# Kernel optimization log

Hardware: AMD Instinct MI355X
Metric: run time of the kernel (lower is better)

Reference implementation:

```python
import jax, jax.numpy as jnp
import numpy as np

N = 256
DT = 1.0 / 4096.0
BATCH = 256
LENGTH = 4096

def _legt_transition(n):
    # HiPPO-LegT continuous-time transition (Gu et al.)
    Q = np.arange(n, dtype=np.float64)
    R = (2.0 * Q + 1.0) ** 0.5
    j, i = np.meshgrid(Q, Q)
    A = R[:, None] * np.where(i < j, (-1.0) ** (i - j), 1.0) * R[None, :]
    B = R[:, None]
    return -A, B

def _bilinear(A, B, dt):
    # scipy cont2discrete(method='bilinear'), alpha=0.5
    n = A.shape[0]
    ima = np.eye(n) - 0.5 * dt * A
    Ad = np.linalg.solve(ima, np.eye(n) + 0.5 * dt * A)
    Bd = np.linalg.solve(ima, dt * B)
    return Ad, Bd

def setup_inputs() -> dict:
    key = jax.random.key(0)
    Ac, Bc = _legt_transition(N)
    evals = (2.0 * np.arange(N, dtype=np.float64) + 1.0) ** 0.5
    C = evals @ Ac                        # (N,) readout from continuous A
    D = np.sum(evals * Bc.squeeze(-1))    # scalar
    scale = 1.0 / (1.0 - 0.5 * D * DT)
    C_discr = (scale * 0.5 * DT * C).astype(np.float32)          # (N,)
    D_discr = np.array([scale * (1.0 + 0.5 * DT * D)], np.float32)  # (1,)
    Ad, Bd = _bilinear(Ac, Bc, DT)
    inputs = jax.random.normal(key, (BATCH, LENGTH), dtype=jnp.float32)
    return {
        "inputs": inputs,
        "A": jnp.asarray(Ad, dtype=jnp.float32),
        "B": jnp.asarray(Bd.squeeze(-1), dtype=jnp.float32),
        "C_discr": jnp.asarray(C_discr),
        "D_discr": jnp.asarray(D_discr),
    }

def reference(inputs, A, B, C_discr, D_discr):
    # inputs: (batch, length). teacher_ratio=1.0 -> fully teacher-forced LTI scan:
    #   c_t = A c_{t-1} + B * u_t ;  pred_t = fac_t * (c_t @ C) + D * u_t
    # where fac_0 = 1 and fac_t = 2 for t > 0 (as in the torch loop).
    batch, length = inputs.shape
    c0 = jnp.zeros((batch, A.shape[0]), dtype=inputs.dtype)
    facs = jnp.where(jnp.arange(length) == 0, 1.0, 2.0).astype(inputs.dtype)

    def step(c, xs):
        x_t, fac = xs                                   # x_t: (batch,)
        c = c @ A.T + B[None, :] * x_t[:, None]         # (batch, N); F.linear(c, A)
        pred = fac * (c @ C_discr) + D_discr[0] * x_t   # (batch,)
        return c, pred

    _, preds = jax.lax.scan(step, c0, (inputs.T, facs))  # preds: (length, batch)
    return preds.T  # (batch, length)
```

## Files before the change

### kernel.cpp

```cpp
#include <hip/hip_runtime.h>


#define LENGTH 4096

#define WS_P2    0
#define WS_P4    65536
#define WS_P8    131072
#define WS_P16   196608
#define WS_P32   262144
#define WS_P64T  327680
#define WS_P128T 393216
#define WS_W     458752
#define WS_V     475136
#define WS_K     491520
#define WS_XH    495616
#define WS_XL    1019904
#define WS_AH    1544192
#define WS_AL    1609728

typedef __attribute__((ext_vector_type(8))) short bf16x8;
typedef __attribute__((ext_vector_type(4))) float f32x4;
#define MFMA(a, b, c) __builtin_amdgcn_mfma_f32_16x16x32_bf16(a, b, c, 0, 0, 0)

__device__ inline unsigned short f2bf(float f) {
    unsigned int u = __float_as_uint(f);
    return (unsigned short)((u + 0x7FFFu + ((u >> 16) & 1u)) >> 16);
}
__device__ inline void split2(float f, short& h, short& l) {
    unsigned short hu = f2bf(f);
    float fh = __uint_as_float((unsigned int)hu << 16);
    h = (short)hu;
    l = (short)f2bf(f - fh);
}

__global__ __launch_bounds__(1024) void mmrow(const float* __restrict__ X,
                                              const float* __restrict__ Y,
                                              float* __restrict__ Z) {
    const int i = blockIdx.x, t = threadIdx.x;
    const int j = t & 255, p = t >> 8;
    __shared__ float red[3][256];
    const float* xr = X + i * 256 + 64 * p;
    const float* yc = Y + (64 * p) * 256 + j;
    float a0 = 0.f, a1 = 0.f, a2 = 0.f, a3 = 0.f;
#pragma unroll
    for (int l = 0; l < 64; l += 4) {
        a0 = fmaf(xr[l + 0], yc[(l + 0) * 256], a0);
        a1 = fmaf(xr[l + 1], yc[(l + 1) * 256], a1);
        a2 = fmaf(xr[l + 2], yc[(l + 2) * 256], a2);
        a3 = fmaf(xr[l + 3], yc[(l + 3) * 256], a3);
    }
    float s = (a0 + a1) + (a2 + a3);
    if (p) red[p - 1][j] = s;
    __syncthreads();
    if (p == 0) Z[i * 256 + j] = s + red[0][j] + red[1][j] + red[2][j];
}

__global__ __launch_bounds__(1024) void mm2(const float* __restrict__ P32,
                                            float* __restrict__ P64T) {
    const int i = blockIdx.x, t = threadIdx.x;
    const int j = t & 255, p = t >> 8;
    __shared__ float red[3][256];
    const float* xr = P32 + i * 256 + 64 * p;
    const float* yc = P32 + (64 * p) * 256 + j;
    float a0 = 0.f, a1 = 0.f, a2 = 0.f, a3 = 0.f;
#pragma unroll
    for (int l = 0; l < 64; l += 4) {
        a0 = fmaf(xr[l + 0], yc[(l + 0) * 256], a0);
        a1 = fmaf(xr[l + 1], yc[(l + 1) * 256], a1);
        a2 = fmaf(xr[l + 2], yc[(l + 2) * 256], a2);
        a3 = fmaf(xr[l + 3], yc[(l + 3) * 256], a3);
    }
    float s = (a0 + a1) + (a2 + a3);
    if (p) red[p - 1][j] = s;
    __syncthreads();
    if (p == 0) P64T[j * 256 + i] = s + red[0][j] + red[1][j] + red[2][j];
}

__global__ __launch_bounds__(1024) void wvgen(const float* __restrict__ A,
                                              const float* __restrict__ B,
                                              const float* __restrict__ C,
                                              const float* __restrict__ P32,
                                              const float* __restrict__ P64T,
                                              const float* __restrict__ P128T,
                                              float* __restrict__ W,
                                              float* __restrict__ V) {
    const int t = threadIdx.x;
    const int bid = blockIdx.x;
    const int j = t & 255, p = t >> 8;
    __shared__ float cur[256];
    __shared__ float red[4][256];

    if (bid < 2) {
        float areg[64];
#pragma unroll
        for (int ii = 0; ii < 64; ++ii) areg[ii] = A[(64 * p + ii) * 256 + j];

        if (bid == 0) {
            if (t < 256) cur[t] = C[t];
            __syncthreads();
        } else {
            float s0 = 0.f, s1 = 0.f, s2 = 0.f, s3 = 0.f;
#pragma unroll 4
            for (int ii = 0; ii < 64; ii += 4) {
                s0 = fmaf(C[64 * p + ii + 0], P32[(64 * p + ii + 0) * 256 + j], s0);
                s1 = fmaf(C[64 * p + ii + 1], P32[(64 * p + ii + 1) * 256 + j], s1);
                s2 = fmaf(C[64 * p + ii + 2], P32[(64 * p + ii + 2) * 256 + j], s2);
                s3 = fmaf(C[64 * p + ii + 3], P32[(64 * p + ii + 3) * 256 + j], s3);
            }
            red[p][j] = (s0 + s1) + (s2 + s3);
            __syncthreads();
            if (p == 0) cur[j] = red[0][j] + red[1][j] + red[2][j] + red[3][j];
            __syncthreads();
        }
        const int base = bid * 32;
        if (p == 0) W[base * 256 + j] = cur[j];
        for (int r = 1; r < 32; ++r) {
            float s0 = 0.f, s1 = 0.f, s2 = 0.f, s3 = 0.f;
#pragma unroll
            for (int m = 0; m < 16; ++m) {
                float4 c4 = *reinterpret_cast<const float4*>(&cur[64 * p + 4 * m]);
                s0 = fmaf(c4.x, areg[4 * m + 0], s0);
                s1 = fmaf(c4.y, areg[4 * m + 1], s1);
                s2 = fmaf(c4.z, areg[4 * m + 2], s2);
                s3 = fmaf(c4.w, areg[4 * m + 3], s3);
            }
            red[p][j] = (s0 + s1) + (s2 + s3);
            __syncthreads();
            if (p == 0) {
                float s = red[0][j] + red[1][j] + red[2][j] + red[3][j];
                cur[j] = s;
                W[(base + r) * 256 + j] = s;
            }
            __syncthreads();
        }
    } else {
        const int i = j;
        float mreg[64];
#pragma unroll
        for (int jj = 0; jj < 64; ++jj) mreg[jj] = P128T[(64 * p + jj) * 256 + i];
        if (t < 256) cur[t] = B[t];
        __syncthreads();

        if (bid == 3) {
            float s0 = 0.f, s1 = 0.f, s2 = 0.f, s3 = 0.f;
#pragma unroll 4
            for (int jj = 0; jj < 64; jj += 4) {
                s0 = fmaf(P64T[(64 * p + jj + 0) * 256 + i], cur[64 * p + jj + 0], s0);
                s1 = fmaf(P64T[(64 * p + jj + 1) * 256 + i], cur[64 * p + jj + 1], s1);
                s2 = fmaf(P64T[(64 * p + jj + 2) * 256 + i], cur[64 * p + jj + 2], s2);
                s3 = fmaf(P64T[(64 * p + jj + 3) * 256 + i], cur[64 * p + jj + 3], s3);
            }
            red[p][i] = (s0 + s1) + (s2 + s3);
            __syncthreads();
            if (p == 0) cur[i] = red[0][i] + red[1][i] + red[2][i] + red[3][i];
            __syncthreads();
        }
        const int off = bid - 2;
        for (int m = 0; m < 32; ++m) {
            if (p == 0) V[(2 * m + off) * 256 + i] = cur[i];
            if (m == 31) break;
            float s0 = 0.f, s1 = 0.f, s2 = 0.f, s3 = 0.f;
#pragma unroll
            for (int mm = 0; mm < 16; ++mm) {
                float4 c4 = *reinterpret_cast<const float4*>(&cur[64 * p + 4 * mm]);
                s0 = fmaf(c4.x, mreg[4 * mm + 0], s0);
                s1 = fmaf(c4.y, mreg[4 * mm + 1], s1);
                s2 = fmaf(c4.z, mreg[4 * mm + 2], s2);
                s3 = fmaf(c4.w, mreg[4 * mm + 3], s3);
            }
            red[p][i] = (s0 + s1) + (s2 + s3);
            __syncthreads();
            if (p == 0) cur[i] = red[0][i] + red[1][i] + red[2][i] + red[3][i];
            __syncthreads();
        }
    }
}

__global__ __launch_bounds__(256) void kdot(const float* __restrict__ W,
                                            const float* __restrict__ V,
                                            float* __restrict__ K) {
    const int q = blockIdx.x, tid = threadIdx.x;
    const int r = tid & 63, p = tid >> 6;
    __shared__ float Wl[64 * 257];
    __shared__ float Vl[256];
    __shared__ float red[4][64];
    for (int u = 0; u < 64; ++u) Wl[u * 257 + tid] = W[u * 256 + tid];
    Vl[tid] = V[q * 256 + tid];
    __syncthreads();
    float s0 = 0.f, s1 = 0.f;
#pragma unroll
    for (int m = 0; m < 64; m += 2) {
        s0 = fmaf(Wl[r * 257 + 64 * p + m + 0], Vl[64 * p + m + 0], s0);
        s1 = fmaf(Wl[r * 257 + 64 * p + m + 1], Vl[64 * p + m + 1], s1);
    }
    red[p][r] = s0 + s1;
    __syncthreads();
    if (tid < 64) K[q * 64 + tid] = red[0][tid] + red[1][tid] + red[2][tid] + red[3][tid];
}

__global__ __launch_bounds__(256) void xsplit(const float* __restrict__ x,
                                              short* __restrict__ XH,
                                              short* __restrict__ XL) {
    const int w = threadIdx.x >> 6, lane = threadIdx.x & 63;
    const int p = blockIdx.x * 4 + w;
    const int c = p >> 4, blk = p & 15;
    const int b = blk * 16 + (lane & 15);
    const int s0 = c * 32 + 8 * (lane >> 4);
    const float4 v0 = reinterpret_cast<const float4*>(&x[b * LENGTH + s0])[0];
    const float4 v1 = reinterpret_cast<const float4*>(&x[b * LENGTH + s0])[1];
    const float f[8] = {v0.x, v0.y, v0.z, v0.w, v1.x, v1.y, v1.z, v1.w};
    bf16x8 hv, lv;
#pragma unroll
    for (int e = 0; e < 8; ++e) {
        short h, l;
        split2(f[e], h, l);
        hv[e] = h; lv[e] = l;
    }
    const int off = (p * 64 + lane) * 8;
    *reinterpret_cast<bf16x8*>(XH + off) = hv;
    *reinterpret_cast<bf16x8*>(XL + off) = lv;
}

__global__ __launch_bounds__(256) void afrag(const float* __restrict__ K,
                                             short* __restrict__ AH,
                                             short* __restrict__ AL) {
    const int m = blockIdx.x * 4 + (threadIdx.x >> 6);
    const int lane = threadIdx.x & 63;
    bf16x8 hv, lv;
#pragma unroll
    for (int e = 0; e < 8; ++e) {
        const int kidx = 16 * m + (lane & 15) - 8 * (lane >> 4) - e;
        const float kv = (kidx >= 0) ? K[kidx] : 0.f;
        short h, l;
        split2(kv, h, l);
        hv[e] = h; lv[e] = l;
    }
    const int off = (m * 64 + lane) * 8;
    *reinterpret_cast<bf16x8*>(AH + off) = hv;
    *reinterpret_cast<bf16x8*>(AL + off) = lv;
}

struct Frag {
    bf16x8 bh0, bh1, bl0, bl1;
    bf16x8 ah0, ah1, ah2, ah3, al0, al1, al2, al3;
    int d0, tile;
};

__global__ __launch_bounds__(512) void convm(const short* __restrict__ XH,
                                             const short* __restrict__ XL,
                                             const short* __restrict__ AH,
                                             const short* __restrict__ AL,
                                             const float* __restrict__ x,
                                             const float* __restrict__ Dp,
                                             float* __restrict__ out) {
    const int pr = blockIdx.x & 31;
    const int bt = blockIdx.x >> 5;
    const int tid = threadIdx.x;
    const int w = tid >> 6, lane = tid & 63;
    const int tA64 = pr * 64, tB64 = (63 - pr) * 64;
    const int nA = 2 * pr + 2;
    const int bt2 = bt * 2;

    __shared__ float lds[16 * 64 * 34];

    f32x4 acc[2][4][2];
#pragma unroll
    for (int t_ = 0; t_ < 2; ++t_)
#pragma unroll
        for (int r_ = 0; r_ < 4; ++r_)
#pragma unroll
            for (int c_ = 0; c_ < 2; ++c_) acc[t_][r_][c_] = f32x4{0.f, 0.f, 0.f, 0.f};

#define LOADF(F, IDX_) do {                                                    \
        const int i_ = (IDX_);                                                 \
        const int tl_ = (i_ < nA) ? 0 : 1;                                     \
        const int cc_ = i_ - (tl_ ? nA : 0);                                   \
        const int xo_ = ((cc_ * 16 + bt2) * 64 + lane) * 8;                    \
        F.bh0 = *reinterpret_cast<const bf16x8*>(XH + xo_);                    \
        F.bh1 = *reinterpret_cast<const bf16x8*>(XH + xo_ + 512);              \
        F.bl0 = *reinterpret_cast<const bf16x8*>(XL + xo_);                    \
        F.bl1 = *reinterpret_cast<const bf16x8*>(XL + xo_ + 512);              \
        const int d_ = (tl_ ? tB64 : tA64) - cc_ * 32;                         \
        F.d0 = d_; F.tile = tl_;                                               \
        const int m0_ = (d_ > 0 ? d_ : 0) >> 4;                                \
        const int m1_ = (d_ + 16 > 0 ? d_ + 16 : 0) >> 4;                      \
        const int m2_ = (d_ + 32 > 0 ? d_ + 32 : 0) >> 4;                      \
        const int m3_ = (d_ + 48 > 0 ? d_ + 48 : 0) >> 4;                      \
        F.ah0 = *reinterpret_cast<const bf16x8*>(AH + (m0_ * 64 + lane) * 8);  \
        F.al0 = *reinterpret_cast<const bf16x8*>(AL + (m0_ * 64 + lane) * 8);  \
        F.ah1 = *reinterpret_cast<const bf16x8*>(AH + (m1_ * 64 + lane) * 8);  \
        F.al1 = *reinterpret_cast<const bf16x8*>(AL + (m1_ * 64 + lane) * 8);  \
        F.ah2 = *reinterpret_cast<const bf16x8*>(AH + (m2_ * 64 + lane) * 8);  \
        F.al2 = *reinterpret_cast<const bf16x8*>(AL + (m2_ * 64 + lane) * 8);  \
        F.ah3 = *reinterpret_cast<const bf16x8*>(AH + (m3_ * 64 + lane) * 8);  \
        F.al3 = *reinterpret_cast<const bf16x8*>(AL + (m3_ * 64 + lane) * 8);  \
    } while (0)

#define ONER(F, T, R, AHF, ALF)                                                \
        if (F.d0 + 16 * R >= 0) {                                              \
            acc[T][R][0] = MFMA(F.AHF, F.bh0, acc[T][R][0]);                   \
            acc[T][R][1] = MFMA(F.AHF, F.bh1, acc[T][R][1]);                   \
            acc[T][R][0] = MFMA(F.AHF, F.bl0, acc[T][R][0]);                   \
            acc[T][R][1] = MFMA(F.AHF, F.bl1, acc[T][R][1]);                   \
            acc[T][R][0] = MFMA(F.ALF, F.bh0, acc[T][R][0]);                   \
            acc[T][R][1] = MFMA(F.ALF, F.bh1, acc[T][R][1]);                   \
        }

#define APPLY(F) do {                                                          \
        if (F.tile == 0) {                                                     \
            ONER(F, 0, 0, ah0, al0) ONER(F, 0, 1, ah1, al1)                    \
            ONER(F, 0, 2, ah2, al2) ONER(F, 0, 3, ah3, al3)                    \
        } else {                                                               \
            ONER(F, 1, 0, ah0, al0) ONER(F, 1, 1, ah1, al1)                    \
            ONER(F, 1, 2, ah2, al2) ONER(F, 1, 3, ah3, al3)                    \
        }                                                                      \
    } while (0)

    Frag f0, f1;
    LOADF(f0, w);
    int idx = w;
    while (true) {
        const int n1 = idx + 8;
        const bool h1 = n1 < 130;
        if (h1) LOADF(f1, n1);
        APPLY(f0);
        if (!h1) break;
        const int n2 = n1 + 8;
        const bool h2 = n2 < 130;
        if (h2) LOADF(f0, n2);
        APPLY(f1);
        if (!h2) break;
        idx = n2;
    }

    const int lq = lane >> 4, lr = lane & 15;
#pragma unroll
    for (int t_ = 0; t_ < 2; ++t_)
#pragma unroll
        for (int r_ = 0; r_ < 4; ++r_)
#pragma unroll
            for (int c_ = 0; c_ < 2; ++c_)
#pragma unroll
                for (int e_ = 0; e_ < 4; ++e_)
                    lds[((w * 2 + t_) * 64 + (r_ * 16 + lq * 4 + e_)) * 34 +
                        (c_ * 16 + lr)] = acc[t_][r_][c_][e_];
    __syncthreads();

    const float D = Dp[0];
    const int b = tid >> 4;
    const int t4 = (tid & 15) * 4;
#pragma unroll
    for (int t_ = 0; t_ < 2; ++t_) {
        const int tbase = t_ ? tB64 : tA64;
        float s0 = 0.f, s1 = 0.f, s2 = 0.f, s3 = 0.f;
#pragma unroll
        for (int w_ = 0; w_ < 8; ++w_) {
            const float* lp = &lds[((w_ * 2 + t_) * 64 + t4) * 34 + b];
            s0 += lp[0]; s1 += lp[34]; s2 += lp[68]; s3 += lp[102];
        }
        const int g = (bt * 32 + b) * LENGTH + tbase + t4;
        const float4 xv = *reinterpret_cast<const float4*>(x + g);
        float4 o;
        o.x = 2.f * s0 + D * xv.x;
        o.y = 2.f * s1 + D * xv.y;
        o.z = 2.f * s2 + D * xv.z;
        o.w = 2.f * s3 + D * xv.w;
        if (tbase == 0 && t4 == 0) o.x -= s0;
        *reinterpret_cast<float4*>(out + g) = o;
    }
}

extern "C" void kernel_launch(void* const* d_in, const int* in_sizes, int n_in,
                              void* d_out, int out_size, void* d_ws, size_t ws_size,
                              hipStream_t stream) {
    const float* x  = (const float*)d_in[0];
    const float* A  = (const float*)d_in[1];
    const float* B  = (const float*)d_in[2];
    const float* C  = (const float*)d_in[3];
    const float* Dp = (const float*)d_in[4];
    float* out = (float*)d_out;
    float* ws  = (float*)d_ws;

    float* P2    = ws + WS_P2;
    float* P4    = ws + WS_P4;
    float* P8    = ws + WS_P8;
    float* P16   = ws + WS_P16;
    float* P32   = ws + WS_P32;
    float* P64T  = ws + WS_P64T;
    float* P128T = ws + WS_P128T;
    float* Wm    = ws + WS_W;
    float* Vm    = ws + WS_V;
    float* K     = ws + WS_K;
    short* XHs   = (short*)(ws + WS_XH);
    short* XLs   = (short*)(ws + WS_XL);
    short* AHs   = (short*)(ws + WS_AH);
    short* ALs   = (short*)(ws + WS_AL);

    xsplit<<<512, 256, 0, stream>>>(x, XHs, XLs);
    mmrow<<<256, 1024, 0, stream>>>(A, A, P2);
    mmrow<<<256, 1024, 0, stream>>>(P2, P2, P4);
    mmrow<<<256, 1024, 0, stream>>>(P4, P4, P8);
    mmrow<<<256, 1024, 0, stream>>>(P8, P8, P16);
    mmrow<<<256, 1024, 0, stream>>>(P16, P16, P32);
    mm2<<<256, 1024, 0, stream>>>(P32, P64T);
    mmrow<<<256, 1024, 0, stream>>>(P64T, P64T, P128T);
    wvgen<<<4, 1024, 0, stream>>>(A, B, C, P32, P64T, P128T, Wm, Vm);
    kdot<<<64, 256, 0, stream>>>(Wm, Vm, K);
    afrag<<<64, 256, 0, stream>>>(K, AHs, ALs);
    convm<<<256, 512, 0, stream>>>(XHs, XLs, AHs, ALs, x, Dp, out);
}
```

Before: 103.8 us.

## Fuse kernel-generation pipeline into one cooperative kernel with grid syncs

Replaces the chain of eleven small launches (xsplit, repeated squaring matmuls, wvgen, kdot, afrag) with one cooperative kernel of 256 blocks that separates phases with grid.sync. If cooperative launch fails it falls back to per-phase launches. It also reworks the W/V generation to use 16-step chains across 4 blocks with an extra P256 power, overlapping that work with the P128/P256 squarings. K computation and fragment packing are fused so K no longer goes through global memory. The aim is to remove launch overhead and serialised low-occupancy phases, at the cost of grid barrier latency and one large kernel with heavy register and shared-memory use.

```diff
diff --git a/kernel.cpp b/kernel.cpp
--- a/kernel.cpp
+++ b/kernel.cpp
@@ -1,4 +1,7 @@
 #include <hip/hip_runtime.h>
+#include <hip/hip_cooperative_groups.h>
+
+namespace cg = cooperative_groups;
 
 
 #define LENGTH 4096
@@ -10,13 +13,13 @@
 #define WS_P32   262144
 #define WS_P64T  327680
 #define WS_P128T 393216
-#define WS_W     458752
-#define WS_V     475136
-#define WS_K     491520
-#define WS_XH    495616
-#define WS_XL    1019904
-#define WS_AH    1544192
-#define WS_AL    1609728
+#define WS_P256T 458752
+#define WS_W     524288
+#define WS_V     540672
+#define WS_XH    557056
+#define WS_XL    1081344
+#define WS_AH    1605632
+#define WS_AL    1671168
 
 typedef __attribute__((ext_vector_type(8))) short bf16x8;
 typedef __attribute__((ext_vector_type(4))) float f32x4;
@@ -33,13 +36,12 @@
     l = (short)f2bf(f - fh);
 }
 
-__global__ __launch_bounds__(1024) void mmrow(const float* __restrict__ X,
-                                              const float* __restrict__ Y,
-                                              float* __restrict__ Z) {
-    const int i = blockIdx.x, t = threadIdx.x;
+__device__ __forceinline__ void mm_body(const float* __restrict__ X,
+                                        const float* __restrict__ Y,
+                                        float* __restrict__ Z,
+                                        int row, int t, bool trans, float* red) {
     const int j = t & 255, p = t >> 8;
-    __shared__ float red[3][256];
-    const float* xr = X + i * 256 + 64 * p;
+    const float* xr = X + row * 256 + 64 * p;
     const float* yc = Y + (64 * p) * 256 + j;
     float a0 = 0.f, a1 = 0.f, a2 = 0.f, a3 = 0.f;
 #pragma unroll
@@ -50,194 +52,255 @@
         a3 = fmaf(xr[l + 3], yc[(l + 3) * 256], a3);
     }
     float s = (a0 + a1) + (a2 + a3);
-    if (p) red[p - 1][j] = s;
-    __syncthreads();
-    if (p == 0) Z[i * 256 + j] = s + red[0][j] + red[1][j] + red[2][j];
-}
-
-__global__ __launch_bounds__(1024) void mm2(const float* __restrict__ P32,
-                                            float* __restrict__ P64T) {
-    const int i = blockIdx.x, t = threadIdx.x;
+    __syncthreads();
+    if (p) red[(p - 1) * 256 + j] = s;
+    __syncthreads();
+    if (!p) {
+        float z = s + red[j] + red[256 + j] + red[512 + j];
+        if (trans) Z[j * 256 + row] = z;
+        else       Z[row * 256 + j] = z;
+    }
+}
+
+__device__ __forceinline__ void rv_mm(const float* __restrict__ v,
+                                      const float* __restrict__ M,
+                                      float* curl, float* red4, int j, int p) {
+    float s0 = 0.f, s1 = 0.f;
+#pragma unroll
+    for (int ii = 0; ii < 64; ii += 2) {
+        s0 = fmaf(v[64 * p + ii],     M[(64 * p + ii) * 256 + j],     s0);
+        s1 = fmaf(v[64 * p + ii + 1], M[(64 * p + ii + 1) * 256 + j], s1);
+    }
+    red4[p * 256 + j] = s0 + s1;
+    __syncthreads();
+    if (!p) curl[j] = red4[j] + red4[256 + j] + red4[512 + j] + red4[768 + j];
+    __syncthreads();
+}
+
+__device__ __forceinline__ void cv_mm(const float* __restrict__ MT,
+                                      const float* __restrict__ v,
+                                      float* curl, float* red4, int i, int p) {
+    float s0 = 0.f, s1 = 0.f;
+#pragma unroll
+    for (int jj = 0; jj < 64; jj += 2) {
+        s0 = fmaf(MT[(64 * p + jj) * 256 + i],     v[64 * p + jj],     s0);
+        s1 = fmaf(MT[(64 * p + jj + 1) * 256 + i], v[64 * p + jj + 1], s1);
+    }
+    red4[p * 256 + i] = s0 + s1;
+    __syncthreads();
+    if (!p) curl[i] = red4[i] + red4[256 + i] + red4[512 + i] + red4[768 + i];
+    __syncthreads();
+}
+
+__global__ __launch_bounds__(1024) void genk(const float* __restrict__ x,
+                                             const float* __restrict__ A,
+                                             const float* __restrict__ B,
+                                             const float* __restrict__ C,
+                                             float* __restrict__ ws,
+                                             int ph) {
+    const bool coop = (ph < 0);
+    cg::grid_group grid = cg::this_grid();
+    const int bid = blockIdx.x;
+    const int t = threadIdx.x;
     const int j = t & 255, p = t >> 8;
-    __shared__ float red[3][256];
-    const float* xr = P32 + i * 256 + 64 * p;
-    const float* yc = P32 + (64 * p) * 256 + j;
-    float a0 = 0.f, a1 = 0.f, a2 = 0.f, a3 = 0.f;
-#pragma unroll
-    for (int l = 0; l < 64; l += 4) {
-        a0 = fmaf(xr[l + 0], yc[(l + 0) * 256], a0);
-        a1 = fmaf(xr[l + 1], yc[(l + 1) * 256], a1);
-        a2 = fmaf(xr[l + 2], yc[(l + 2) * 256], a2);
-        a3 = fmaf(xr[l + 3], yc[(l + 3) * 256], a3);
-    }
-    float s = (a0 + a1) + (a2 + a3);
-    if (p) red[p - 1][j] = s;
-    __syncthreads();
-    if (p == 0) P64T[j * 256 + i] = s + red[0][j] + red[1][j] + red[2][j];
-}
-
-__global__ __launch_bounds__(1024) void wvgen(const float* __restrict__ A,
-                                              const float* __restrict__ B,
-                                              const float* __restrict__ C,
-                                              const float* __restrict__ P32,
-                                              const float* __restrict__ P64T,
-                                              const float* __restrict__ P128T,
-                                              float* __restrict__ W,
-                                              float* __restrict__ V) {
-    const int t = threadIdx.x;
-    const int bid = blockIdx.x;
-    const int j = t & 255, p = t >> 8;
-    __shared__ float cur[256];
-    __shared__ float red[4][256];
-
-    if (bid < 2) {
-        float areg[64];
-#pragma unroll
-        for (int ii = 0; ii < 64; ++ii) areg[ii] = A[(64 * p + ii) * 256 + j];
-
-        if (bid == 0) {
-            if (t < 256) cur[t] = C[t];
+
+    __shared__ __align__(16) float shm[17376];
+    float* red  = shm;
+    float* curl = shm + 1024;
+    float* red4 = shm + 1280;
+
+    float* P2    = ws + WS_P2;
+    float* P4    = ws + WS_P4;
+    float* P8    = ws + WS_P8;
+    float* P16   = ws + WS_P16;
+    float* P32   = ws + WS_P32;
+    float* P64T  = ws + WS_P64T;
+    float* P128T = ws + WS_P128T;
+    float* P256T = ws + WS_P256T;
+    float* Wm    = ws + WS_W;
+    float* Vm    = ws + WS_V;
+    short* XH    = (short*)(ws + WS_XH);
+    short* XL    = (short*)(ws + WS_XL);
+    short* AH    = (short*)(ws + WS_AH);
+    short* AL    = (short*)(ws + WS_AL);
+
+    if (coop || ph == 0) {
+        mm_body(A, A, P2, bid, t, false, red);
+        const int wv = t >> 6, lane = t & 63;
+        if (wv < 8) {
+            const int pj = bid * 8 + wv;
+            const int c = pj >> 4, blk = pj & 15;
+            const int b = blk * 16 + (lane & 15);
+            const int s0 = c * 32 + 8 * (lane >> 4);
+            const float4 v0 = reinterpret_cast<const float4*>(&x[b * LENGTH + s0])[0];
+            const float4 v1 = reinterpret_cast<const float4*>(&x[b * LENGTH + s0])[1];
+            const float f[8] = {v0.x, v0.y, v0.z, v0.w, v1.x, v1.y, v1.z, v1.w};
+            bf16x8 hv, lv;
+#pragma unroll
+            for (int e = 0; e < 8; ++e) {
+                short h_, l_;
+                split2(f[e], h_, l_);
+                hv[e] = h_; lv[e] = l_;
+            }
+            const int off = (pj * 64 + lane) * 8;
+            *reinterpret_cast<bf16x8*>(XH + off) = hv;
+            *reinterpret_cast<bf16x8*>(XL + off) = lv;
+        }
+    }
+    if (coop) grid.sync();
+    if (coop || ph == 1) mm_body(P2, P2, P4, bid, t, false, red);
+    if (coop) grid.sync();
+    if (coop || ph == 2) mm_body(P4, P4, P8, bid, t, false, red);
+    if (coop) grid.sync();
+    if (coop || ph == 3) mm_body(P8, P8, P16, bid, t, false, red);
+    if (coop) grid.sync();
+    if (coop || ph == 4) mm_body(P16, P16, P32, bid, t, false, red);
+    if (coop) grid.sync();
+    if (coop || ph == 5) mm_body(P32, P32, P64T, bid, t, true, red);
+    if (coop) grid.sync();
+
+    if (coop || ph == 6) {
+        if (bid >= 4) {
+            mm_body(P64T, P64T, P128T, bid - 4, t, false, red);
+            if (bid < 8) mm_body(P64T, P64T, P128T, 248 + bid, t, false, red);
+        } else {
+            const int c = bid;
+            float areg[64];
+#pragma unroll
+            for (int ii = 0; ii < 64; ++ii) areg[ii] = A[(64 * p + ii) * 256 + j];
+            if (c == 0) {
+                if (t < 256) curl[t] = C[t];
+                __syncthreads();
+            } else {
+                rv_mm(C, (c == 2) ? P32 : P16, curl, red4, j, p);
+                if (c == 3) rv_mm(curl, P32, curl, red4, j, p);
+            }
+            for (int s_ = 0; s_ < 16; ++s_) {
+                if (!p) Wm[(16 * c + s_) * 256 + j] = curl[j];
+                if (s_ == 15) break;
+                float s0 = 0.f, s1 = 0.f;
+#pragma unroll
+                for (int m = 0; m < 16; ++m) {
+                    float4 c4 = *reinterpret_cast<const float4*>(&curl[64 * p + 4 * m]);
+                    s0 = fmaf(c4.x, areg[4 * m + 0], s0);
+                    s1 = fmaf(c4.y, areg[4 * m + 1], s1);
+                    s0 = fmaf(c4.z, areg[4 * m + 2], s0);
+                    s1 = fmaf(c4.w, areg[4 * m + 3], s1);
+                }
+                red4[p * 256 + j] = s0 + s1;
+                __syncthreads();
+                if (!p) curl[j] = red4[j] + red4[256 + j] + red4[512 + j] + red4[768 + j];
+                __syncthreads();
+            }
+        }
+    }
+    if (coop) grid.sync();
+
+    if (coop || ph == 7) {
+        if (bid >= 4) {
+            mm_body(P128T, P128T, P256T, bid - 4, t, false, red);
+            if (bid < 8) mm_body(P128T, P128T, P256T, 248 + bid, t, false, red);
+        } else {
+            const int c = bid;
+            if (c == 0) {
+                if (t < 256) Vm[t] = B[t];
+            } else if (c == 1) {
+                cv_mm(P64T, B, curl, red4, j, p);
+                if (!p) Vm[256 + j] = curl[j];
+            } else if (c == 2) {
+                cv_mm(P128T, B, curl, red4, j, p);
+                if (!p) Vm[512 + j] = curl[j];
+            } else {
+                cv_mm(P128T, B, curl, red4, j, p);
+                cv_mm(P64T, curl, curl, red4, j, p);
+                if (!p) Vm[768 + j] = curl[j];
+            }
+        }
+    }
+    if (coop) grid.sync();
+
+    if (coop || ph == 8) {
+        if (bid < 4) {
+            const int c = bid, i = j;
+            if (t < 256) curl[t] = Vm[c * 256 + t];
             __syncthreads();
-        } else {
-            float s0 = 0.f, s1 = 0.f, s2 = 0.f, s3 = 0.f;
-#pragma unroll 4
-            for (int ii = 0; ii < 64; ii += 4) {
-                s0 = fmaf(C[64 * p + ii + 0], P32[(64 * p + ii + 0) * 256 + j], s0);
-                s1 = fmaf(C[64 * p + ii + 1], P32[(64 * p + ii + 1) * 256 + j], s1);
-                s2 = fmaf(C[64 * p + ii + 2], P32[(64 * p + ii + 2) * 256 + j], s2);
-                s3 = fmaf(C[64 * p + ii + 3], P32[(64 * p + ii + 3) * 256 + j], s3);
-            }
-            red[p][j] = (s0 + s1) + (s2 + s3);
+            float mreg[64];
+#pragma unroll
+            for (int jj = 0; jj < 64; ++jj) mreg[jj] = P256T[(64 * p + jj) * 256 + i];
+            for (int s_ = 1; s_ < 16; ++s_) {
+                float s0 = 0.f, s1 = 0.f;
+#pragma unroll
+                for (int m = 0; m < 16; ++m) {
+                    float4 c4 = *reinterpret_cast<const float4*>(&curl[64 * p + 4 * m]);
+                    s0 = fmaf(c4.x, mreg[4 * m + 0], s0);
+                    s1 = fmaf(c4.y, mreg[4 * m + 1], s1);
+                    s0 = fmaf(c4.z, mreg[4 * m + 2], s0);
+                    s1 = fmaf(c4.w, mreg[4 * m + 3], s1);
+                }
+                red4[p * 256 + i] = s0 + s1;
+                __syncthreads();
+                if (!p) {
+                    float s = red4[i] + red4[256 + i] + red4[512 + i] + red4[768 + i];
+                    curl[i] = s;
+                    Vm[(4 * s_ + c) * 256 + i] = s;
+                }
+                __syncthreads();
+            }
+        }
+    }
+    if (coop) grid.sync();
+
+    if (coop || ph == 9) {
+        if (bid < 32) {
+            float* Wl = shm;
+            float* Vl = shm + 16448;
+            float* kl = shm + 17216;
+            for (int u = t; u < 16384; u += 1024)
+                Wl[(u >> 8) * 257 + (u & 255)] = Wm[u];
+            if (t < 768) {
+                const int q = 2 * bid - 1 + (t >> 8);
+                Vl[t] = (q >= 0) ? Vm[q * 256 + (t & 255)] : 0.f;
+            }
             __syncthreads();
-            if (p == 0) cur[j] = red[0][j] + red[1][j] + red[2][j] + red[3][j];
+            if (t < 143) {
+                const int tau = 128 * bid - 15 + t;
+                float s = 0.f;
+                if (tau >= 0) {
+                    const int r = tau & 63;
+                    const int qq = (tau >> 6) - (2 * bid - 1);
+                    const float* wr = &Wl[r * 257];
+                    const float* vr = &Vl[qq * 256];
+                    float s0 = 0.f, s1 = 0.f, s2 = 0.f, s3 = 0.f;
+#pragma unroll 8
+                    for (int i2 = 0; i2 < 256; i2 += 4) {
+                        s0 = fmaf(wr[i2 + 0], vr[i2 + 0], s0);
+                        s1 = fmaf(wr[i2 + 1], vr[i2 + 1], s1);
+                        s2 = fmaf(wr[i2 + 2], vr[i2 + 2], s2);
+                        s3 = fmaf(wr[i2 + 3], vr[i2 + 3], s3);
+                    }
+                    s = (s0 + s1) + (s2 + s3);
+                }
+                kl[t] = s;
+            }
             __syncthreads();
-        }
-        const int base = bid * 32;
-        if (p == 0) W[base * 256 + j] = cur[j];
-        for (int r = 1; r < 32; ++r) {
-            float s0 = 0.f, s1 = 0.f, s2 = 0.f, s3 = 0.f;
-#pragma unroll
-            for (int m = 0; m < 16; ++m) {
-                float4 c4 = *reinterpret_cast<const float4*>(&cur[64 * p + 4 * m]);
-                s0 = fmaf(c4.x, areg[4 * m + 0], s0);
-                s1 = fmaf(c4.y, areg[4 * m + 1], s1);
-                s2 = fmaf(c4.z, areg[4 * m + 2], s2);
-                s3 = fmaf(c4.w, areg[4 * m + 3], s3);
-            }
-            red[p][j] = (s0 + s1) + (s2 + s3);
-            __syncthreads();
-            if (p == 0) {
-                float s = red[0][j] + red[1][j] + red[2][j] + red[3][j];
-                cur[j] = s;
-                W[(base + r) * 256 + j] = s;
-            }
-            __syncthreads();
-        }
-    } else {
-        const int i = j;
-        float mreg[64];
-#pragma unroll
-        for (int jj = 0; jj < 64; ++jj) mreg[jj] = P128T[(64 * p + jj) * 256 + i];
-        if (t < 256) cur[t] = B[t];
-        __syncthreads();
-
-        if (bid == 3) {
-            float s0 = 0.f, s1 = 0.f, s2 = 0.f, s3 = 0.f;
-#pragma unroll 4
-            for (int jj = 0; jj < 64; jj += 4) {
-                s0 = fmaf(P64T[(64 * p + jj + 0) * 256 + i], cur[64 * p + jj + 0], s0);
-                s1 = fmaf(P64T[(64 * p + jj + 1) * 256 + i], cur[64 * p + jj + 1], s1);
-                s2 = fmaf(P64T[(64 * p + jj + 2) * 256 + i], cur[64 * p + jj + 2], s2);
-                s3 = fmaf(P64T[(64 * p + jj + 3) * 256 + i], cur[64 * p + jj + 3], s3);
-            }
-            red[p][i] = (s0 + s1) + (s2 + s3);
-            __syncthreads();
-            if (p == 0) cur[i] = red[0][i] + red[1][i] + red[2][i] + red[3][i];
-            __syncthreads();
-        }
-        const int off = bid - 2;
-        for (int m = 0; m < 32; ++m) {
-            if (p == 0) V[(2 * m + off) * 256 + i] = cur[i];
-            if (m == 31) break;
-            float s0 = 0.f, s1 = 0.f, s2 = 0.f, s3 = 0.f;
-#pragma unroll
-            for (int mm = 0; mm < 16; ++mm) {
-                float4 c4 = *reinterpret_cast<const float4*>(&cur[64 * p + 4 * mm]);
-                s0 = fmaf(c4.x, mreg[4 * mm + 0], s0);
-                s1 = fmaf(c4.y, mreg[4 * mm + 1], s1);
-                s2 = fmaf(c4.z, mreg[4 * mm + 2], s2);
-                s3 = fmaf(c4.w, mreg[4 * mm + 3], s3);
-            }
-            red[p][i] = (s0 + s1) + (s2 + s3);
-            __syncthreads();
-            if (p == 0) cur[i] = red[0][i] + red[1][i] + red[2][i] + red[3][i];
-            __syncthreads();
-        }
-    }
-}
-
-__global__ __launch_bounds__(256) void kdot(const float* __restrict__ W,
-                                            const float* __restrict__ V,
-                                            float* __restrict__ K) {
-    const int q = blockIdx.x, tid = threadIdx.x;
-    const int r = tid & 63, p = tid >> 6;
-    __shared__ float Wl[64 * 257];
-    __shared__ float Vl[256];
-    __shared__ float red[4][64];
-    for (int u = 0; u < 64; ++u) Wl[u * 257 + tid] = W[u * 256 + tid];
-    Vl[tid] = V[q * 256 + tid];
-    __syncthreads();
-    float s0 = 0.f, s1 = 0.f;
-#pragma unroll
-    for (int m = 0; m < 64; m += 2) {
-        s0 = fmaf(Wl[r * 257 + 64 * p + m + 0], Vl[64 * p + m + 0], s0);
-        s1 = fmaf(Wl[r * 257 + 64 * p + m + 1], Vl[64 * p + m + 1], s1);
-    }
-    red[p][r] = s0 + s1;
-    __syncthreads();
-    if (tid < 64) K[q * 64 + tid] = red[0][tid] + red[1][tid] + red[2][tid] + red[3][tid];
-}
-
-__global__ __launch_bounds__(256) void xsplit(const float* __restrict__ x,
-                                              short* __restrict__ XH,
-                                              short* __restrict__ XL) {
-    const int w = threadIdx.x >> 6, lane = threadIdx.x & 63;
-    const int p = blockIdx.x * 4 + w;
-    const int c = p >> 4, blk = p & 15;
-    const int b = blk * 16 + (lane & 15);
-    const int s0 = c * 32 + 8 * (lane >> 4);
-    const float4 v0 = reinterpret_cast<const float4*>(&x[b * LENGTH + s0])[0];
-    const float4 v1 = reinterpret_cast<const float4*>(&x[b * LENGTH + s0])[1];
-    const float f[8] = {v0.x, v0.y, v0.z, v0.w, v1.x, v1.y, v1.z, v1.w};
-    bf16x8 hv, lv;
-#pragma unroll
-    for (int e = 0; e < 8; ++e) {
-        short h, l;
-        split2(f[e], h, l);
-        hv[e] = h; lv[e] = l;
-    }
-    const int off = (p * 64 + lane) * 8;
-    *reinterpret_cast<bf16x8*>(XH + off) = hv;
-    *reinterpret_cast<bf16x8*>(XL + off) = lv;
-}
-
-__global__ __launch_bounds__(256) void afrag(const float* __restrict__ K,
-                                             short* __restrict__ AH,
-                                             short* __restrict__ AL) {
-    const int m = blockIdx.x * 4 + (threadIdx.x >> 6);
-    const int lane = threadIdx.x & 63;
-    bf16x8 hv, lv;
-#pragma unroll
-    for (int e = 0; e < 8; ++e) {
-        const int kidx = 16 * m + (lane & 15) - 8 * (lane >> 4) - e;
-        const float kv = (kidx >= 0) ? K[kidx] : 0.f;
-        short h, l;
-        split2(kv, h, l);
-        hv[e] = h; lv[e] = l;
-    }
-    const int off = (m * 64 + lane) * 8;
-    *reinterpret_cast<bf16x8*>(AH + off) = hv;
-    *reinterpret_cast<bf16x8*>(AL + off) = lv;
+            const int wv = t >> 6, lane = t & 63;
+            if (wv < 8) {
+                const int m = 8 * bid + wv;
+                bf16x8 hv, lv;
+#pragma unroll
+                for (int el = 0; el < 8; ++el) {
+                    const int rel = 16 * wv + (lane & 15) - 8 * (lane >> 4) - el + 15;
+                    const float kv = (rel >= 0) ? kl[rel] : 0.f;
+                    short h_, l_;
+                    split2(kv, h_, l_);
+                    hv[el] = h_; lv[el] = l_;
+                }
+                const int off = (m * 64 + lane) * 8;
+                *reinterpret_cast<bf16x8*>(AH + off) = hv;
+                *reinterpret_cast<bf16x8*>(AL + off) = lv;
+            }
+        }
+    }
 }
 
 struct Frag {
@@ -245,31 +308,6 @@
     bf16x8 ah0, ah1, ah2, ah3, al0, al1, al2, al3;
     int d0, tile;
 };
-
-__global__ __launch_bounds__(512) void convm(const short* __restrict__ XH,
-                                             const short* __restrict__ XL,
-                                             const short* __restrict__ AH,
-                                             const short* __restrict__ AL,
-                                             const float* __restrict__ x,
-                                             const float* __restrict__ Dp,
-                                             float* __restrict__ out) {
-    const int pr = blockIdx.x & 31;
-    const int bt = blockIdx.x >> 5;
-    const int tid = threadIdx.x;
-    const int w = tid >> 6, lane = tid & 63;
-    const int tA64 = pr * 64, tB64 = (63 - pr) * 64;
-    const int nA = 2 * pr + 2;
-    const int bt2 = bt * 2;
-
-    __shared__ float lds[16 * 64 * 34];
-
-    f32x4 acc[2][4][2];
-#pragma unroll
-    for (int t_ = 0; t_ < 2; ++t_)
-#pragma unroll
-        for (int r_ = 0; r_ < 4; ++r_)
-#pragma unroll
-            for (int c_ = 0; c_ < 2; ++c_) acc[t_][r_][c_] = f32x4{0.f, 0.f, 0.f, 0.f};
 
 #define LOADF(F, IDX_) do {                                                    \
         const int i_ = (IDX_);                                                 \
@@ -316,6 +354,31 @@
         }                                                                      \
     } while (0)
 
+__global__ __launch_bounds__(512) void convm(const short* __restrict__ XH,
+                                             const short* __restrict__ XL,
+                                             const short* __restrict__ AH,
+                                             const short* __restrict__ AL,
+                                             const float* __restrict__ x,
+                                             const float* __restrict__ Dp,
+                                             float* __restrict__ out) {
+    const int pr = blockIdx.x & 31;
+    const int bt = blockIdx.x >> 5;
+    const int tid = threadIdx.x;
+    const int w = tid >> 6, lane = tid & 63;
+    const int tA64 = pr * 64, tB64 = (63 - pr) * 64;
+    const int nA = 2 * pr + 2;
+    const int bt2 = bt * 2;
+
+    __shared__ float lds[16 * 64 * 34];
+
+    f32x4 acc[2][4][2];
+#pragma unroll
+    for (int t_ = 0; t_ < 2; ++t_)
+#pragma unroll
+        for (int r_ = 0; r_ < 4; ++r_)
+#pragma unroll
+            for (int c_ = 0; c_ < 2; ++c_) acc[t_][r_][c_] = f32x4{0.f, 0.f, 0.f, 0.f};
+
     Frag f0, f1;
     LOADF(f0, w);
     int idx = w;
@@ -381,31 +444,18 @@
     float* out = (float*)d_out;
     float* ws  = (float*)d_ws;
 
-    float* P2    = ws + WS_P2;
-    float* P4    = ws + WS_P4;
-    float* P8    = ws + WS_P8;
-    float* P16   = ws + WS_P16;
-    float* P32   = ws + WS_P32;
-    float* P64T  = ws + WS_P64T;
-    float* P128T = ws + WS_P128T;
-    float* Wm    = ws + WS_W;
-    float* Vm    = ws + WS_V;
-    float* K     = ws + WS_K;
-    short* XHs   = (short*)(ws + WS_XH);
-    short* XLs   = (short*)(ws + WS_XL);
-    short* AHs   = (short*)(ws + WS_AH);
-    short* ALs   = (short*)(ws + WS_AL);
-
-    xsplit<<<512, 256, 0, stream>>>(x, XHs, XLs);
-    mmrow<<<256, 1024, 0, stream>>>(A, A, P2);
-    mmrow<<<256, 1024, 0, stream>>>(P2, P2, P4);
-    mmrow<<<256, 1024, 0, stream>>>(P4, P4, P8);
-    mmrow<<<256, 1024, 0, stream>>>(P8, P8, P16);
-    mmrow<<<256, 1024, 0, stream>>>(P16, P16, P32);
-    mm2<<<256, 1024, 0, stream>>>(P32, P64T);
-    mmrow<<<256, 1024, 0, stream>>>(P64T, P64T, P128T);
-    wvgen<<<4, 1024, 0, stream>>>(A, B, C, P32, P64T, P128T, Wm, Vm);
-    kdot<<<64, 256, 0, stream>>>(Wm, Vm, K);
-    afrag<<<64, 256, 0, stream>>>(K, AHs, ALs);
+    short* XHs = (short*)(ws + WS_XH);
+    short* XLs = (short*)(ws + WS_XL);
+    short* AHs = (short*)(ws + WS_AH);
+    short* ALs = (short*)(ws + WS_AL);
+
+    int ph = -1;
+    void* args[] = {(void*)&x, (void*)&A, (void*)&B, (void*)&C, (void*)&ws, (void*)&ph};
+    hipError_t e = hipLaunchCooperativeKernel((const void*)genk, dim3(256), dim3(1024),
+                                              args, 0, stream);
+    if (e != hipSuccess) {
+        for (int i = 0; i <= 9; ++i)
+            genk<<<256, 1024, 0, stream>>>(x, A, B, C, ws, i);
+    }
     convm<<<256, 512, 0, stream>>>(XHs, XLs, AHs, ALs, x, Dp, out);
 }
```

Result: slower. 366.8 us (+253.2%).
